# Performance work log

Hardware: AMD Instinct MI355X
Metric: run time of the kernel (lower is better)

## Reference

```python
import jax, jax.numpy as jnp
import numpy as np

NUM_HEADS = 16

def _rope_tables(seq_len, dim, dtype):
    # LongLlamaRotaryEmbedding: inv_freq = 1/10000^(2i/d), emb = cat(freqs, freqs)
    inv_freq = 1.0 / (10000.0 ** (jnp.arange(0, dim, 2, dtype=jnp.float32) / dim))
    t = jnp.arange(seq_len, dtype=jnp.float32)
    freqs = t[:, None] * inv_freq[None, :]            # [S, D/2]
    emb = jnp.concatenate([freqs, freqs], axis=-1)    # [S, D]
    return jnp.cos(emb).astype(dtype), jnp.sin(emb).astype(dtype)

def _rotate_half(x):
    x1, x2 = jnp.split(x, 2, axis=-1)
    return jnp.concatenate([-x2, x1], axis=-1)

def _rotate_one(x, cos, sin, pos):
    # x: [B,H,S,D]; pos: [B,S] int -> gather-indexed RoPE
    c = cos[pos][:, None, :, :]  # [B,1,S,D]
    s = sin[pos][:, None, :, :]
    return x * c + _rotate_half(x) * s

def setup_inputs() -> dict:
    key = jax.random.key(0)
    B, S, HID = 1, 4096, 2048
    ks = jax.random.split(key, 5)
    hidden_states = jax.random.normal(ks[0], (B, S, HID), dtype=jnp.float32)
    # causal additive mask [B,1,S,S]: 0 where allowed, large negative above diagonal
    causal = jnp.tril(jnp.ones((S, S), dtype=bool))
    attention_mask = jnp.where(causal, 0.0, -1e9).astype(jnp.float32)[None, None]
    attention_mask = jnp.broadcast_to(attention_mask, (B, 1, S, S))
    position_ids = jnp.broadcast_to(jnp.arange(S, dtype=jnp.int64), (B, S))
    scale = 0.02
    Wq = jax.random.normal(ks[1], (HID, HID), dtype=jnp.float32) * scale
    Wk = jax.random.normal(ks[2], (HID, HID), dtype=jnp.float32) * scale
    Wv = jax.random.normal(ks[3], (HID, HID), dtype=jnp.float32) * scale
    Wo = jax.random.normal(ks[4], (HID, HID), dtype=jnp.float32) * scale
    return {"hidden_states": hidden_states, "attention_mask": attention_mask,
            "position_ids": position_ids, "Wq": Wq, "Wk": Wk, "Wv": Wv, "Wo": Wo}

def reference(hidden_states, attention_mask, position_ids, Wq, Wk, Wv, Wo):
    B, S, HID = hidden_states.shape
    H = NUM_HEADS
    D = HID // H
    # QKV projections (torch Linear: y = x @ W.T), shaped [B,H,S,D]
    q = (hidden_states @ Wq.T).reshape(B, S, H, D).transpose(0, 2, 1, 3)
    k = (hidden_states @ Wk.T).reshape(B, S, H, D).transpose(0, 2, 1, 3)
    v = (hidden_states @ Wv.T).reshape(B, S, H, D).transpose(0, 2, 1, 3)
    kv_seq_len = k.shape[-2]
    cos, sin = _rope_tables(kv_seq_len, D, hidden_states.dtype)
    # rel_pos_ids = position_ids - min over seq (gather-indexed RoPE)
    rel = position_ids - jnp.min(position_ids, axis=-1, keepdims=True)
    q = _rotate_one(q, cos, sin, rel[:, -S:])
    k = _rotate_one(k, cos, sin, rel)
    scores = jnp.einsum('bhqd,bhkd->bhqk', q, k) / jnp.asarray(np.sqrt(D), hidden_states.dtype)
    scores = scores + attention_mask  # additive mask broadcast over heads
    attn = jax.nn.softmax(scores, axis=-1)
    out = jnp.einsum('bhqk,bhkd->bhqd', attn, v)
    out = out.transpose(0, 2, 1, 3).reshape(B, S, HID)
    return out @ Wo.T
```

## Files before the change

kernel.cpp:

```cpp
#include <hip/hip_runtime.h>
#include <stdint.h>

typedef uint16_t u16;
typedef __bf16 bf16x8 __attribute__((ext_vector_type(8)));
typedef float f32x4 __attribute__((ext_vector_type(4)));
typedef uint32_t u32x4 __attribute__((ext_vector_type(4)));

__device__ __forceinline__ u16 f2bf(float f) {
    uint32_t u = __builtin_bit_cast(uint32_t, f);
    u += 0x7fffu + ((u >> 16) & 1u);
    return (u16)(u >> 16);
}
__device__ __forceinline__ float bf2f(u16 h) {
    uint32_t u = ((uint32_t)h) << 16;
    return __builtin_bit_cast(float, u);
}

__global__ __launch_bounds__(256) void cvt_f32_bf16(const float* __restrict__ in,
                                                    u16* __restrict__ out, int n4) {
    int i = blockIdx.x * 256 + threadIdx.x;
    if (i >= n4) return;
    float4 v = ((const float4*)in)[i];
    u16 o[4] = { f2bf(v.x), f2bf(v.y), f2bf(v.z), f2bf(v.w) };
    *(uint64_t*)(out + 4 * (size_t)i) = *(const uint64_t*)o;
}

__global__ __launch_bounds__(256) void cvt_w4(const float* __restrict__ W0,
                                              const float* __restrict__ W1,
                                              const float* __restrict__ W2,
                                              const float* __restrict__ W3,
                                              u16* __restrict__ Wqkv,
                                              u16* __restrict__ Wob) {
    int b = blockIdx.x;
    int w = b >> 12;
    const float* in = (w == 0 ? W0 : w == 1 ? W1 : w == 2 ? W2 : W3);
    u16* out = (w < 3 ? Wqkv + (size_t)w * 4194304 : Wob);
    int i = (b & 4095) * 256 + threadIdx.x;
    float4 v = ((const float4*)in)[i];
    u16 o[4] = { f2bf(v.x), f2bf(v.y), f2bf(v.z), f2bf(v.w) };
    *(uint64_t*)(out + 4 * (size_t)i) = *(const uint64_t*)o;
}

__device__ __forceinline__ void gload16(const u16* g, u16* l) {
    __builtin_amdgcn_global_load_lds(
        (const __attribute__((address_space(1))) void*)g,
        (__attribute__((address_space(3))) void*)l, 16, 0, 0);
}

__global__ __launch_bounds__(512, 1) void gemm_qkv(const u16* __restrict__ A,
                                                   const u16* __restrict__ B,
                                                   u16* __restrict__ Cq,
                                                   int K) {
    __shared__ u16 As[2][16384];
    __shared__ u16 Bs[2][12288];
    const int tid  = threadIdx.x;
    const int wave = tid >> 6, lane = tid & 63;
    const int quad = lane >> 4, ln = lane & 15;
    const int wm = wave >> 2, wn = wave & 3;
    const int bm = blockIdx.x, bn = blockIdx.y;
    const int NT = K >> 6;
    const u16* Ab = A + (size_t)bm * 256 * K;
    const u16* Bb = B + (size_t)bn * 192 * K;
    const int lr  = lane >> 3;
    const int lc8 = ((lane & 7) ^ lr) * 8;
    const int sw  = ln & 7;
    const int cA0 = ((0 + quad) ^ sw) * 8;
    const int cA1 = ((4 + quad) ^ sw) * 8;

    f32x4 acc[8][3] = {};

    auto stage_a = [&](int t, int q) {
        int ch = q * 8 + wave;
        gload16(Ab + (size_t)(ch * 8 + lr) * K + t * 64 + lc8, &As[t & 1][ch * 512]);
    };
    auto stage_b = [&](int t, int q) {
        int ch = q * 8 + wave;
        gload16(Bb + (size_t)(ch * 8 + lr) * K + t * 64 + lc8, &Bs[t & 1][ch * 512]);
    };

    for (int q = 0; q < 4; q++) stage_a(0, q);
    for (int q = 0; q < 3; q++) stage_b(0, q);
    for (int q = 0; q < 4; q++) stage_a(1, q);
    asm volatile("s_waitcnt vmcnt(4)" ::: "memory");
    __builtin_amdgcn_s_barrier();

    for (int t = 0; t < NT; ++t) {
        const u16* Asb = As[t & 1];
        const u16* Bsb = Bs[t & 1];
        bf16x8 a0[8], a1[8], b0[3], b1[3];
#pragma unroll
        for (int i = 0; i < 8; i++)
            a0[i] = *(const bf16x8*)(Asb + (wm * 128 + i * 16 + ln) * 64 + cA0);
#pragma unroll
        for (int j = 0; j < 3; j++)
            b0[j] = *(const bf16x8*)(Bsb + (wn * 48 + j * 16 + ln) * 64 + cA0);
        if (t + 1 < NT) { stage_b(t + 1, 0); stage_b(t + 1, 1); }
        __builtin_amdgcn_s_barrier();
        asm volatile("s_waitcnt lgkmcnt(0)" ::: "memory");
        __builtin_amdgcn_s_setprio(1);
#pragma unroll
        for (int i = 0; i < 4; i++)
#pragma unroll
            for (int j = 0; j < 3; j++)
                acc[i][j] = __builtin_amdgcn_mfma_f32_16x16x32_bf16(a0[i], b0[j], acc[i][j], 0, 0, 0);
        __builtin_amdgcn_s_setprio(0);
        __builtin_amdgcn_s_barrier();
#pragma unroll
        for (int i = 0; i < 8; i++)
            a1[i] = *(const bf16x8*)(Asb + (wm * 128 + i * 16 + ln) * 64 + cA1);
#pragma unroll
        for (int j = 0; j < 3; j++)
            b1[j] = *(const bf16x8*)(Bsb + (wn * 48 + j * 16 + ln) * 64 + cA1);
        if (t + 1 < NT) stage_b(t + 1, 2);
        __builtin_amdgcn_s_barrier();
        asm volatile("s_waitcnt lgkmcnt(0)" ::: "memory");
        __builtin_amdgcn_s_setprio(1);
#pragma unroll
        for (int i = 4; i < 8; i++)
#pragma unroll
            for (int j = 0; j < 3; j++)
                acc[i][j] = __builtin_amdgcn_mfma_f32_16x16x32_bf16(a0[i], b0[j], acc[i][j], 0, 0, 0);
        __builtin_amdgcn_s_setprio(0);
        __builtin_amdgcn_s_barrier();
        if (t + 2 < NT) { stage_a(t + 2, 0); stage_a(t + 2, 1); }
        __builtin_amdgcn_s_barrier();
        __builtin_amdgcn_s_setprio(1);
#pragma unroll
        for (int i = 0; i < 4; i++)
#pragma unroll
            for (int j = 0; j < 3; j++)
                acc[i][j] = __builtin_amdgcn_mfma_f32_16x16x32_bf16(a1[i], b1[j], acc[i][j], 0, 0, 0);
        __builtin_amdgcn_s_setprio(0);
        __builtin_amdgcn_s_barrier();
        if (t + 2 < NT) { stage_a(t + 2, 2); stage_a(t + 2, 3); }
        __builtin_amdgcn_s_barrier();
        __builtin_amdgcn_s_setprio(1);
#pragma unroll
        for (int i = 4; i < 8; i++)
#pragma unroll
            for (int j = 0; j < 3; j++)
                acc[i][j] = __builtin_amdgcn_mfma_f32_16x16x32_bf16(a1[i], b1[j], acc[i][j], 0, 0, 0);
        __builtin_amdgcn_s_setprio(0);
        asm volatile("s_waitcnt vmcnt(4)" ::: "memory");
        __builtin_amdgcn_s_barrier();
    }
#pragma unroll
    for (int i = 0; i < 8; i++) {
        size_t row0 = (size_t)(bm * 256 + wm * 128 + i * 16 + quad * 4);
#pragma unroll
        for (int j = 0; j < 3; j++) {
            int n = bn * 192 + wn * 48 + j * 16 + ln;
            size_t off = ((size_t)(n >> 11) << 23) + (size_t)(n & 2047);
#pragma unroll
            for (int r = 0; r < 4; r++)
                Cq[off + (row0 + r) * 2048] = f2bf(acc[i][j][r]);
        }
    }
}

__global__ __launch_bounds__(256, 2) void gemm_o(const u16* __restrict__ A,
                                                 const u16* __restrict__ B,
                                                 float* __restrict__ C,
                                                 int K) {
    __shared__ u16 As[2][8192];
    __shared__ u16 Bs[2][8192];
    const int tid  = threadIdx.x;
    const int wave = tid >> 6, lane = tid & 63;
    const int quad = lane >> 4, ln = lane & 15;
    const int wm = (wave & 1) * 64, wn = (wave >> 1) * 64;
    const int bm = blockIdx.x, bn = blockIdx.y;
    const int NT = K >> 6;
    const u16* Ab = A + (size_t)bm * 128 * K;
    const u16* Bb = B + (size_t)bn * 128 * K;
    const int lr  = lane >> 3;
    const int lc8 = ((lane & 7) ^ lr) * 8;
    const int sw  = ln & 7;
    const int cA0 = ((0 + quad) ^ sw) * 8;
    const int cA1 = ((4 + quad) ^ sw) * 8;

    f32x4 acc[4][4] = {};

    auto stage_a = [&](int t, int q) {
        int ch = q * 4 + wave;
        gload16(Ab + (size_t)(ch * 8 + lr) * K + t * 64 + lc8, &As[t & 1][ch * 512]);
    };
    auto stage_b = [&](int t, int q) {
        int ch = q * 4 + wave;
        gload16(Bb + (size_t)(ch * 8 + lr) * K + t * 64 + lc8, &Bs[t & 1][ch * 512]);
    };

    for (int q = 0; q < 4; q++) stage_a(0, q);
    for (int q = 0; q < 4; q++) stage_b(0, q);
    for (int q = 0; q < 4; q++) stage_a(1, q);
    asm volatile("s_waitcnt vmcnt(4)" ::: "memory");
    __builtin_amdgcn_s_barrier();

    for (int t = 0; t < NT; ++t) {
        const u16* Asb = As[t & 1];
        const u16* Bsb = Bs[t & 1];
        bf16x8 a0[4], a1[4], b0[4], b1[4];
#pragma unroll
        for (int i = 0; i < 4; i++) {
            a0[i] = *(const bf16x8*)(Asb + (wm + i * 16 + ln) * 64 + cA0);
            b0[i] = *(const bf16x8*)(Bsb + (wn + i * 16 + ln) * 64 + cA0);
        }
        if (t + 1 < NT) { stage_b(t + 1, 0); stage_b(t + 1, 1); }
        __builtin_amdgcn_s_barrier();
        asm volatile("s_waitcnt lgkmcnt(0)" ::: "memory");
        __builtin_amdgcn_s_setprio(1);
#pragma unroll
        for (int i = 0; i < 2; i++)
#pragma unroll
            for (int j = 0; j < 4; j++)
                acc[i][j] = __builtin_amdgcn_mfma_f32_16x16x32_bf16(a0[i], b0[j], acc[i][j], 0, 0, 0);
        __builtin_amdgcn_s_setprio(0);
        __builtin_amdgcn_s_barrier();
#pragma unroll
        for (int i = 0; i < 4; i++) {
            a1[i] = *(const bf16x8*)(Asb + (wm + i * 16 + ln) * 64 + cA1);
            b1[i] = *(const bf16x8*)(Bsb + (wn + i * 16 + ln) * 64 + cA1);
        }
        if (t + 1 < NT) { stage_b(t + 1, 2); stage_b(t + 1, 3); }
        __builtin_amdgcn_s_barrier();
        asm volatile("s_waitcnt lgkmcnt(0)" ::: "memory");
        __builtin_amdgcn_s_setprio(1);
#pragma unroll
        for (int i = 2; i < 4; i++)
#pragma unroll
            for (int j = 0; j < 4; j++)
                acc[i][j] = __builtin_amdgcn_mfma_f32_16x16x32_bf16(a0[i], b0[j], acc[i][j], 0, 0, 0);
        __builtin_amdgcn_s_setprio(0);
        __builtin_amdgcn_s_barrier();
        if (t + 2 < NT) { stage_a(t + 2, 0); stage_a(t + 2, 1); }
        __builtin_amdgcn_s_barrier();
        __builtin_amdgcn_s_setprio(1);
#pragma unroll
        for (int i = 0; i < 2; i++)
#pragma unroll
            for (int j = 0; j < 4; j++)
                acc[i][j] = __builtin_amdgcn_mfma_f32_16x16x32_bf16(a1[i], b1[j], acc[i][j], 0, 0, 0);
        __builtin_amdgcn_s_setprio(0);
        __builtin_amdgcn_s_barrier();
        if (t + 2 < NT) { stage_a(t + 2, 2); stage_a(t + 2, 3); }
        __builtin_amdgcn_s_barrier();
        __builtin_amdgcn_s_setprio(1);
#pragma unroll
        for (int i = 2; i < 4; i++)
#pragma unroll
            for (int j = 0; j < 4; j++)
                acc[i][j] = __builtin_amdgcn_mfma_f32_16x16x32_bf16(a1[i], b1[j], acc[i][j], 0, 0, 0);
        __builtin_amdgcn_s_setprio(0);
        if (t + 2 < NT) asm volatile("s_waitcnt vmcnt(4)" ::: "memory");
        else            asm volatile("s_waitcnt vmcnt(0)" ::: "memory");
        __builtin_amdgcn_s_barrier();
    }
#pragma unroll
    for (int i = 0; i < 4; i++)
#pragma unroll
        for (int j = 0; j < 4; j++)
#pragma unroll
            for (int r = 0; r < 4; r++) {
                size_t row = (size_t)(bm * 128 + wm + i * 16 + quad * 4 + r);
                size_t col = (size_t)(bn * 128 + wn + j * 16 + ln);
                C[row * 2048 + col] = acc[i][j][r];
            }
}

__global__ __launch_bounds__(256) void rope_scale(u16* __restrict__ Qb,
                                                  u16* __restrict__ Kb) {
    int idx = blockIdx.x * 256 + threadIdx.x;
    int s   = idx >> 11;
    int rem = idx & 2047;
    int mat = rem >> 10;
    int h   = (rem >> 6) & 15;
    int j   = rem & 63;
    u16* base = (mat ? Kb : Qb) + (size_t)s * 2048 + h * 128;
    float x1 = bf2f(base[j]);
    float x2 = bf2f(base[j + 64]);
    float invf = exp2f((float)(-j) * 0.2076205059304601f);
    float th = (float)s * invf;
    float sn, cs;
    sincosf(th, &sn, &cs);
    float o1 = x1 * cs - x2 * sn;
    float o2 = x2 * cs + x1 * sn;
    const float QS = 0.08838834764831845f * 1.4426950408889634f;
    if (mat == 0) { o1 *= QS; o2 *= QS; }
    base[j]      = f2bf(o1);
    base[j + 64] = f2bf(o2);
}

__global__ __launch_bounds__(256) void transpose_v(const u16* __restrict__ V,
                                                   u16* __restrict__ Vt) {
    const int h  = blockIdx.y;
    const int s0 = blockIdx.x * 64;
    const int tid = threadIdx.x;
    for (int c = tid; c < 1024; c += 256) {
        int d = c >> 3, sc = c & 7;
        u16 tmp[8];
#pragma unroll
        for (int j = 0; j < 8; j++)
            tmp[j] = V[(size_t)(s0 + sc * 8 + j) * 2048 + h * 128 + d];
        *(u32x4*)(Vt + ((size_t)h * 128 + d) * 4096 + s0 + sc * 8) = *(const u32x4*)tmp;
    }
}

__global__ __launch_bounds__(256, 3) void fattn(const u16* __restrict__ Qb,
                                                const u16* __restrict__ Kb,
                                                const u16* __restrict__ Vt,
                                                float* __restrict__ Oacc,
                                                float* __restrict__ Lacc) {
    __shared__ u16 Ks[2][32 * 128];
    __shared__ u16 Vs[2][128 * 32];
    __shared__ u16 Ps[128][40];
    const int tid  = threadIdx.x, wave = tid >> 6, lane = tid & 63;
    const int quad = lane >> 4, ln = lane & 15;
    const int h = blockIdx.x;
    const int y = blockIdx.y;
    int c, qt;
    if (y < 32)      { c = 0; qt = 31 - y; }
    else if (y < 56) { c = 1; qt = 63 - y; }
    else if (y < 72) { c = 2; qt = 87 - y; }
    else             { c = 3; qt = 103 - y; }
    const int q0 = qt * 128;
    const int nkt = min(32, 4 * qt + 4 - 32 * c);
    const int ktbase = 32 * c;

    const u16* Kp0 = Kb + h * 128;
    const u16* Vp0 = Vt + (size_t)h * 128 * 4096;

    bf16x8 aq[2][4];
    const u16* Qp = Qb + (size_t)q0 * 2048 + h * 128;
#pragma unroll
    for (int i = 0; i < 2; i++)
#pragma unroll
        for (int ks = 0; ks < 4; ks++)
            aq[i][ks] = *(const bf16x8*)(Qp + (size_t)(wave * 32 + i * 16 + ln) * 2048
                                         + ks * 32 + quad * 8);

    f32x4 o[2][8] = {};
    float lreg[2][4] = {};

    auto stage = [&](int kt, int b) {
        const u16* Kp = Kp0 + (size_t)(kt * 32) * 2048;
        const u16* Vp = Vp0 + kt * 32;
#pragma unroll
        for (int t = 0; t < 2; t++) {
            int p = (wave * 2 + t) * 64 + lane;
            int r = p >> 4, jc = (p & 15) ^ (r & 15);
            gload16(Kp + (size_t)r * 2048 + jc * 8, &Ks[b][(wave * 2 + t) * 512]);
        }
#pragma unroll
        for (int t = 0; t < 2; t++) {
            int p = (wave * 2 + t) * 64 + lane;
            int r = p >> 2, jc = (p & 3) ^ (r & 3);
            gload16(Vp + (size_t)r * 4096 + jc * 8, &Vs[b][(wave * 2 + t) * 512]);
        }
    };

    stage(ktbase, 0);
    for (int t = 0; t < nkt; t++) {
        __syncthreads();
        if (t + 1 < nkt) stage(ktbase + t + 1, (t + 1) & 1);
        const u16* Ksb = Ks[t & 1];
        const u16* Vsb = Vs[t & 1];

        f32x4 sc[2][2] = {};
        __builtin_amdgcn_s_setprio(1);
#pragma unroll
        for (int ks = 0; ks < 4; ks++)
#pragma unroll
            for (int j = 0; j < 2; j++) {
                int r = j * 16 + ln;
                bf16x8 bk = *(const bf16x8*)(Ksb + (size_t)(r * 16 + ((ks * 4 + quad) ^ ln)) * 8);
                sc[0][j] = __builtin_amdgcn_mfma_f32_16x16x32_bf16(aq[0][ks], bk, sc[0][j], 0, 0, 0);
                sc[1][j] = __builtin_amdgcn_mfma_f32_16x16x32_bf16(aq[1][ks], bk, sc[1][j], 0, 0, 0);
            }
        __builtin_amdgcn_s_setprio(0);
        const int kv0 = (ktbase + t) * 32;
        if (kv0 + 31 > q0 + wave * 32) {
#pragma unroll
            for (int j = 0; j < 2; j++) {
                int col = kv0 + j * 16 + ln;
#pragma unroll
                for (int i = 0; i < 2; i++)
#pragma unroll
                    for (int r = 0; r < 4; r++) {
                        int row = q0 + wave * 32 + i * 16 + quad * 4 + r;
                        if (col > row) sc[i][j][r] = -1e30f;
                    }
            }
        }
#pragma unroll
        for (int i = 0; i < 2; i++)
#pragma unroll
            for (int r = 0; r < 4; r++) {
                float p0 = __builtin_amdgcn_exp2f(sc[i][0][r]);
                float p1 = __builtin_amdgcn_exp2f(sc[i][1][r]);
                lreg[i][r] += p0 + p1;
                int row = wave * 32 + i * 16 + quad * 4 + r;
                Ps[row][ln]      = f2bf(p0);
                Ps[row][16 + ln] = f2bf(p1);
            }
        bf16x8 pa0 = *(const bf16x8*)&Ps[wave * 32 + ln][quad * 8];
        bf16x8 pa1 = *(const bf16x8*)&Ps[wave * 32 + 16 + ln][quad * 8];
        __builtin_amdgcn_s_setprio(1);
#pragma unroll
        for (int n = 0; n < 8; n++) {
            int rv = n * 16 + ln;
            bf16x8 vb = *(const bf16x8*)(Vsb + (size_t)(rv * 4 + (quad ^ (ln & 3))) * 8);
            o[0][n] = __builtin_amdgcn_mfma_f32_16x16x32_bf16(pa0, vb, o[0][n], 0, 0, 0);
            o[1][n] = __builtin_amdgcn_mfma_f32_16x16x32_bf16(pa1, vb, o[1][n], 0, 0, 0);
        }
        __builtin_amdgcn_s_setprio(0);
    }
    float* Op = Oacc + (size_t)(q0 + wave * 32) * 2048 + h * 128;
#pragma unroll
    for (int i = 0; i < 2; i++)
#pragma unroll
        for (int r = 0; r < 4; r++) {
            float l = lreg[i][r];
            l += __shfl_xor(l, 1);
            l += __shfl_xor(l, 2);
            l += __shfl_xor(l, 4);
            l += __shfl_xor(l, 8);
            int row = i * 16 + quad * 4 + r;
            if (ln == 0)
                unsafeAtomicAdd(&Lacc[(size_t)(q0 + wave * 32 + row) * 16 + h], l);
#pragma unroll
            for (int n = 0; n < 8; n++)
                unsafeAtomicAdd(&Op[(size_t)row * 2048 + n * 16 + ln], o[i][n][r]);
        }
}

__global__ __launch_bounds__(256) void attn_norm(const float* __restrict__ Oacc,
                                                 const float* __restrict__ Lacc,
                                                 u16* __restrict__ attn) {
    int i = blockIdx.x * 256 + threadIdx.x;
    int s  = i >> 9;
    int c4 = (i & 511) * 4;
    int h  = c4 >> 7;
    float inv = 1.0f / Lacc[(size_t)s * 16 + h];
    float4 v = ((const float4*)(Oacc + (size_t)s * 2048))[i & 511];
    u16 o[4] = { f2bf(v.x * inv), f2bf(v.y * inv), f2bf(v.z * inv), f2bf(v.w * inv) };
    *(uint64_t*)(attn + (size_t)s * 2048 + c4) = *(const uint64_t*)o;
}

extern "C" void kernel_launch(void* const* d_in, const int* in_sizes, int n_in,
                              void* d_out, int out_size, void* d_ws, size_t ws_size,
                              hipStream_t stream) {
    const float* hs = (const float*)d_in[0];
    const float* Wq = (const float*)d_in[3];
    const float* Wk = (const float*)d_in[4];
    const float* Wv = (const float*)d_in[5];
    const float* Wo = (const float*)d_in[6];

    char* ws = (char*)d_ws;
    u16* Xb   = (u16*)ws;
    u16* Wob  = (u16*)(ws + (size_t)16777216);
    u16* Qb   = (u16*)(ws + (size_t)25165824);
    u16* Kb   = (u16*)(ws + (size_t)41943040);
    u16* Vb   = (u16*)(ws + (size_t)58720256);
    u16* Wqkv = (u16*)(ws + (size_t)75497472);
    u16* Vtg  = (u16*)(ws + (size_t)100663296);
    float* Oacc = (float*)(ws + (size_t)58720256);
    float* Lacc = (float*)(ws + (size_t)92274688);
    u16* attn = Xb;

    cvt_f32_bf16<<<8192, 256, 0, stream>>>(hs, Xb, 2097152);
    cvt_w4<<<16384, 256, 0, stream>>>(Wq, Wk, Wv, Wo, Wqkv, Wob);

    gemm_qkv<<<dim3(16, 32), 512, 0, stream>>>(Xb, Wqkv, Qb, 2048);
    rope_scale<<<32768, 256, 0, stream>>>(Qb, Kb);
    transpose_v<<<dim3(64, 16), 256, 0, stream>>>(Vb, Vtg);
    hipMemsetAsync(Oacc, 0, 33816576, stream);
    fattn<<<dim3(16, 80), 256, 0, stream>>>(Qb, Kb, Vtg, Oacc, Lacc);
    attn_norm<<<8192, 256, 0, stream>>>(Oacc, Lacc, attn);
    gemm_o<<<dim3(32, 16), 256, 0, stream>>>(attn, Wob, (float*)d_out, 2048);
}
```

Measured before the change: 485.9 us.

## Amortize RoPE sincos across heads, LDS-tiled V transpose, raise fattn occupancy

The RoPE kernel now has each thread compute sin/cos once per (position, frequency) and apply it to all 16 heads of both Q and K, cutting transcendental work and launch count. The V transpose stages a 64x128 tile in shared memory so global reads and writes are both coalesced 16-byte accesses, replacing strided 2-byte gathers. The flash-attention kernel drops the padding on the P tile and asks for 4 blocks per SM instead of 3. The unpadded P tile may cause LDS bank conflicts, and the tighter launch bound may force register spills.

```diff
diff --git a/kernel.cpp b/kernel.cpp
--- a/kernel.cpp
+++ b/kernel.cpp
@@ -268,50 +268,66 @@
 
 __global__ __launch_bounds__(256) void rope_scale(u16* __restrict__ Qb,
                                                   u16* __restrict__ Kb) {
-    int idx = blockIdx.x * 256 + threadIdx.x;
-    int s   = idx >> 11;
-    int rem = idx & 2047;
-    int mat = rem >> 10;
-    int h   = (rem >> 6) & 15;
-    int j   = rem & 63;
-    u16* base = (mat ? Kb : Qb) + (size_t)s * 2048 + h * 128;
-    float x1 = bf2f(base[j]);
-    float x2 = bf2f(base[j + 64]);
+    const int j = threadIdx.x & 63;
+    const int s = blockIdx.x * 4 + (threadIdx.x >> 6);
     float invf = exp2f((float)(-j) * 0.2076205059304601f);
     float th = (float)s * invf;
     float sn, cs;
     sincosf(th, &sn, &cs);
-    float o1 = x1 * cs - x2 * sn;
-    float o2 = x2 * cs + x1 * sn;
     const float QS = 0.08838834764831845f * 1.4426950408889634f;
-    if (mat == 0) { o1 *= QS; o2 *= QS; }
-    base[j]      = f2bf(o1);
-    base[j + 64] = f2bf(o2);
+    const float csq = cs * QS, snq = sn * QS;
+    u16* qrow = Qb + (size_t)s * 2048 + j;
+    u16* krow = Kb + (size_t)s * 2048 + j;
+#pragma unroll
+    for (int h = 0; h < 16; h++) {
+        float x1 = bf2f(qrow[h * 128]);
+        float x2 = bf2f(qrow[h * 128 + 64]);
+        qrow[h * 128]      = f2bf(x1 * csq - x2 * snq);
+        qrow[h * 128 + 64] = f2bf(x2 * csq + x1 * snq);
+        float y1 = bf2f(krow[h * 128]);
+        float y2 = bf2f(krow[h * 128 + 64]);
+        krow[h * 128]      = f2bf(y1 * cs - y2 * sn);
+        krow[h * 128 + 64] = f2bf(y2 * cs + y1 * sn);
+    }
 }
 
 __global__ __launch_bounds__(256) void transpose_v(const u16* __restrict__ V,
                                                    u16* __restrict__ Vt) {
+    __shared__ u16 T[64][136];
     const int h  = blockIdx.y;
     const int s0 = blockIdx.x * 64;
     const int tid = threadIdx.x;
-    for (int c = tid; c < 1024; c += 256) {
-        int d = c >> 3, sc = c & 7;
-        u16 tmp[8];
-#pragma unroll
-        for (int j = 0; j < 8; j++)
-            tmp[j] = V[(size_t)(s0 + sc * 8 + j) * 2048 + h * 128 + d];
-        *(u32x4*)(Vt + ((size_t)h * 128 + d) * 4096 + s0 + sc * 8) = *(const u32x4*)tmp;
-    }
-}
-
-__global__ __launch_bounds__(256, 3) void fattn(const u16* __restrict__ Qb,
+    const int sr = tid >> 2, ck = (tid & 3) * 32;
+    const u16* src = V + (size_t)(s0 + sr) * 2048 + h * 128 + ck;
+    u32x4 v0 = *(const u32x4*)(src);
+    u32x4 v1 = *(const u32x4*)(src + 8);
+    u32x4 v2 = *(const u32x4*)(src + 16);
+    u32x4 v3 = *(const u32x4*)(src + 24);
+    *(u32x4*)&T[sr][ck]      = v0;
+    *(u32x4*)&T[sr][ck + 8]  = v1;
+    *(u32x4*)&T[sr][ck + 16] = v2;
+    *(u32x4*)&T[sr][ck + 24] = v3;
+    __syncthreads();
+    const int d = tid >> 1, hs = (tid & 1) * 32;
+    u16 tmp[32];
+#pragma unroll
+    for (int sidx = 0; sidx < 32; sidx++)
+        tmp[sidx] = T[hs + sidx][d];
+    u16* dst = Vt + ((size_t)h * 128 + d) * 4096 + s0 + hs;
+    *(u32x4*)(dst)      = *(const u32x4*)(tmp);
+    *(u32x4*)(dst + 8)  = *(const u32x4*)(tmp + 8);
+    *(u32x4*)(dst + 16) = *(const u32x4*)(tmp + 16);
+    *(u32x4*)(dst + 24) = *(const u32x4*)(tmp + 24);
+}
+
+__global__ __launch_bounds__(256, 4) void fattn(const u16* __restrict__ Qb,
                                                 const u16* __restrict__ Kb,
                                                 const u16* __restrict__ Vt,
                                                 float* __restrict__ Oacc,
                                                 float* __restrict__ Lacc) {
     __shared__ u16 Ks[2][32 * 128];
     __shared__ u16 Vs[2][128 * 32];
-    __shared__ u16 Ps[128][40];
+    __shared__ u16 Ps[128][32];
     const int tid  = threadIdx.x, wave = tid >> 6, lane = tid & 63;
     const int quad = lane >> 4, ln = lane & 15;
     const int h = blockIdx.x;
@@ -470,7 +486,7 @@
     cvt_w4<<<16384, 256, 0, stream>>>(Wq, Wk, Wv, Wo, Wqkv, Wob);
 
     gemm_qkv<<<dim3(16, 32), 512, 0, stream>>>(Xb, Wqkv, Qb, 2048);
-    rope_scale<<<32768, 256, 0, stream>>>(Qb, Kb);
+    rope_scale<<<1024, 256, 0, stream>>>(Qb, Kb);
     transpose_v<<<dim3(64, 16), 256, 0, stream>>>(Vb, Vtg);
     hipMemsetAsync(Oacc, 0, 33816576, stream);
     fattn<<<dim3(16, 80), 256, 0, stream>>>(Qb, Kb, Vtg, Oacc, Lacc);
```

Result: slower. 586.1 us (+20.6%).
